# Performance work log

Measured on AMD Instinct MI355X. Metric: run time of the kernel, lower is better.

Reference implementation:

```python
import jax, jax.numpy as jnp
import numpy as np

R = 64          # n_rois
B = 128         # batch_size (graphs)
IN = 2048       # voxels per ROI
HID = 512       # max(32, IN//4)
ROI_OUT = 20
G1, G2 = 64, 128
FC1, FC2, OUT = 512, 1024, 6400
N = R * B       # total graph nodes


def _block_complete_edges():
    # per-sample complete directed graph over R ROIs (no self loops)
    r = np.arange(R)
    s, d = np.meshgrid(r, r, indexing='ij')
    m = s != d
    s, d = s[m], d[m]                       # [R*(R-1)]
    off = (np.arange(B) * R)[:, None]       # [B,1]
    src = (s[None, :] + off).reshape(-1)
    dst = (d[None, :] + off).reshape(-1)
    return np.stack([src, dst]).astype(np.int64)  # [2, E]


def setup_inputs() -> dict:
    key = jax.random.key(0)
    ks = jax.random.split(key, 16)
    sd = lambda *s: 1.0 / np.sqrt(s[0])
    inp = {
        'x': jax.random.normal(ks[0], (R, B * IN), jnp.float32),
        'edge_index': jnp.asarray(_block_complete_edges()),
        'batch': jnp.repeat(jnp.arange(B, dtype=jnp.int64), R),
        # per-ROI MLP params (batched over ROI axis)
        'W1': jax.random.normal(ks[1], (R, IN, HID), jnp.float32) * sd(IN),
        'b1': jnp.zeros((R, HID), jnp.float32),
        'W2': jax.random.normal(ks[2], (R, HID, ROI_OUT), jnp.float32) * sd(HID),
        'b2': jnp.zeros((R, ROI_OUT), jnp.float32),
        # GCN params
        'Wg1': jax.random.normal(ks[3], (ROI_OUT, G1), jnp.float32) * sd(ROI_OUT),
        'bg1': jnp.zeros((G1,), jnp.float32),
        'Wg2': jax.random.normal(ks[4], (G1, G2), jnp.float32) * sd(G1),
        'bg2': jnp.zeros((G2,), jnp.float32),
        # FC stack
        'Wf1': jax.random.normal(ks[5], (G2, FC1), jnp.float32) * sd(G2),
        'bf1': jnp.zeros((FC1,), jnp.float32),
        'Wf2': jax.random.normal(ks[6], (FC1, FC2), jnp.float32) * sd(FC1),
        'bf2': jnp.zeros((FC2,), jnp.float32),
        'Wo': jax.random.normal(ks[7], (FC2, OUT), jnp.float32) * sd(FC2),
        'bo': jnp.zeros((OUT,), jnp.float32),
    }
    return inp


def _gcn(h, src, dst, W, b):
    # PyG GCNConv: symmetric norm with self loops, then linear
    loop = jnp.arange(N)
    s = jnp.concatenate([src, loop])
    d = jnp.concatenate([dst, loop])
    deg = jax.ops.segment_sum(jnp.ones(s.shape[0], h.dtype), d, num_segments=N)
    dinv = jax.lax.rsqrt(deg)  # deg >= 1 due to self loops
    hw = h @ W                                  # [N, out]
    msg = hw[s] * (dinv[s] * dinv[d])[:, None]  # [E+N, out]
    return jax.ops.segment_sum(msg, d, num_segments=N) + b


def reference(x, edge_index, batch, W1, b1, W2, b2, Wg1, bg1, Wg2, bg2,
              Wf1, bf1, Wf2, bf2, Wo, bo):
    # per-ROI MLPs, batched: x[r] holds B contiguous chunks of IN voxels
    xr = x.reshape(R, B, IN)
    h = jax.nn.relu(jnp.einsum('rbi,rih->rbh', xr, W1) + b1[:, None, :])
    f = jnp.einsum('rbh,rho->rbo', h, W2) + b2[:, None, :]   # [R,B,ROI_OUT]
    # node order in torch code: for b: for r -> node = b*R + r
    node_feats = f.transpose(1, 0, 2).reshape(N, ROI_OUT)

    src, dst = edge_index[0], edge_index[1]
    g = jax.nn.relu(_gcn(node_feats, src, dst, Wg1, bg1))
    g = jax.nn.relu(_gcn(g, src, dst, Wg2, bg2))

    # global mean pool over each graph's R nodes
    pooled = jax.ops.segment_sum(g, batch, num_segments=B) / R  # [B, G2]

    y = jax.nn.relu(pooled @ Wf1 + bf1)
    y = jax.nn.relu(y @ Wf2 + bf2)
    return y @ Wo + bo  # [B, OUT]
```

## Files before the change

kernel.cpp:

```cpp
#include <hip/hip_runtime.h>
#include <hip/hip_bf16.h>
#include <cstdint>

typedef float  f32x4 __attribute__((ext_vector_type(4)));
typedef short  s16x4 __attribute__((ext_vector_type(4)));
typedef short  s16x8 __attribute__((ext_vector_type(8)));
typedef __bf16 bf16x8 __attribute__((ext_vector_type(8)));
typedef unsigned int u32x2 __attribute__((ext_vector_type(2)));
typedef unsigned int u32x4 __attribute__((ext_vector_type(4)));

static __device__ __forceinline__ unsigned short f2bf(float f) {
  union { float f; unsigned u; } v; v.f = f;
  unsigned r = v.u + 0x7fffu + ((v.u >> 16) & 1u);
  return (unsigned short)(r >> 16);
}

static __device__ __forceinline__ unsigned pk2(float lo, float hi) {
  unsigned r;
  asm("v_cvt_pk_bf16_f32 %0, %1, %2" : "=v"(r) : "v"(lo), "v"(hi));
  return r;
}

static __device__ __forceinline__ f32x4 mfma16(bf16x8 a, bf16x8 b, f32x4 c) {
  return __builtin_amdgcn_mfma_f32_16x16x32_bf16(a, b, c, 0, 0, 0);
}

__global__ __launch_bounds__(512, 4)
void k_mlp(const float* __restrict__ X, const float* __restrict__ W1,
           const float* __restrict__ b1, const float* __restrict__ W2,
           float* __restrict__ m1)
{
  __shared__ short smem[21760];
  __shared__ float biasS[128];
  short* const lds_a  = smem;
  short* const lds_b  = smem + 9216;
  short* const lds_h  = smem;
  short* const lds_w2 = smem + 17408;

  const int bid = blockIdx.x;
  const int r = (bid & 7) + ((bid >> 5) << 3);
  const int c = (bid >> 3) & 3;

  const float* xr = X + (long)r * (128 * 2048);
  const float* wr = W1 + (long)r * (2048 * 512) + c * 128;
  const float* bp = b1 + (long)r * 512 + c * 128;

  const int t = threadIdx.x;
  const int lane = t & 63;
  const int w = t >> 6;

  if (t < 128) biasS[t] = bp[t];

  const int aRow = t >> 2;
  const int aCol = (t & 3) * 4;
  const int bn   = t & 127;
  const int bk0  = (t >> 7) * 8;

  f32x4 aR[4];
  float bR[2][8];

  auto loadTile = [&](int ks) {
    const float* xp = xr + (long)aRow * 2048 + ks * 64 + aCol;
#pragma unroll
    for (int j = 0; j < 4; j++)
      aR[j] = *(const f32x4*)(xp + 16 * j);
    const float* wp = wr + (long)(ks * 64 + bk0) * 512 + bn;
#pragma unroll
    for (int g = 0; g < 2; g++)
#pragma unroll
      for (int j = 0; j < 8; j++)
        bR[g][j] = wp[(long)(g * 32 + j) * 512];
  };

  auto storeTile = [&]() {
#pragma unroll
    for (int j = 0; j < 4; j++) {
      u32x2 v;
      v[0] = pk2(aR[j][0], aR[j][1]);
      v[1] = pk2(aR[j][2], aR[j][3]);
      *(u32x2*)&lds_a[aRow * 72 + aCol + 16 * j] = v;
    }
#pragma unroll
    for (int g = 0; g < 2; g++) {
      u32x4 v;
      v[0] = pk2(bR[g][0], bR[g][1]);
      v[1] = pk2(bR[g][2], bR[g][3]);
      v[2] = pk2(bR[g][4], bR[g][5]);
      v[3] = pk2(bR[g][6], bR[g][7]);
      *(u32x4*)&lds_b[bn * 72 + bk0 + g * 32] = v;
    }
  };

  const int wm = w & 1, wn = w >> 1;
  const int mBase = wm * 64, nBase = wn * 32;
  const int lm = lane & 15, lg = lane >> 4;

  f32x4 acc[4][2];
#pragma unroll
  for (int i = 0; i < 4; i++)
#pragma unroll
    for (int j = 0; j < 2; j++) acc[i][j] = f32x4{0.f, 0.f, 0.f, 0.f};

  loadTile(0);
  for (int ks = 0; ks < 32; ks++) {
    __syncthreads();
    storeTile();
    __syncthreads();
    if (ks + 1 < 32) loadTile(ks + 1);
    bf16x8 af[2][4], bfr[2][2];
#pragma unroll
    for (int g = 0; g < 2; g++) {
#pragma unroll
      for (int i = 0; i < 4; i++)
        af[g][i] = *(const bf16x8*)&lds_a[(mBase + i * 16 + lm) * 72 + g * 32 + lg * 8];
#pragma unroll
      for (int j = 0; j < 2; j++)
        bfr[g][j] = *(const bf16x8*)&lds_b[(nBase + j * 16 + lm) * 72 + g * 32 + lg * 8];
    }
#pragma unroll
    for (int mi = 0; mi < 4; mi++)
#pragma unroll
      for (int ni = 0; ni < 2; ni++) {
        acc[mi][ni] = mfma16(af[0][mi], bfr[0][ni], acc[mi][ni]);
        acc[mi][ni] = mfma16(af[1][mi], bfr[1][ni], acc[mi][ni]);
      }
  }

  __syncthreads();

#pragma unroll
  for (int mi = 0; mi < 4; mi++)
#pragma unroll
    for (int ni = 0; ni < 2; ni++) {
      const int col = nBase + ni * 16 + lm;
      const float bv = biasS[col];
#pragma unroll
      for (int i = 0; i < 4; i++) {
        const int row = mBase + mi * 16 + lg * 4 + i;
        float v = acc[mi][ni][i] + bv;
        v = v > 0.f ? v : 0.f;
        lds_h[row * 136 + col] = (short)f2bf(v);
      }
    }
  {
    const float* w2r = W2 + (long)r * (512 * 20) + (long)(c * 128) * 20;
#pragma unroll
    for (int i = 0; i < 8; i++) {
      const int idx = t * 8 + i;
      const int o = idx >> 7, kh = idx & 127;
      const float v = (o < 20) ? w2r[(long)kh * 20 + o] : 0.f;
      lds_w2[o * 136 + kh] = (short)f2bf(v);
    }
  }
  __syncthreads();
  f32x4 acc2[2];
  acc2[0] = f32x4{0.f, 0.f, 0.f, 0.f};
  acc2[1] = f32x4{0.f, 0.f, 0.f, 0.f};
#pragma unroll
  for (int ks2 = 0; ks2 < 4; ks2++) {
    bf16x8 a0 = *(const bf16x8*)&lds_h[(w * 16 + lm) * 136 + ks2 * 32 + lg * 8];
    bf16x8 b0 = *(const bf16x8*)&lds_w2[lm * 136 + ks2 * 32 + lg * 8];
    bf16x8 b1v = *(const bf16x8*)&lds_w2[(16 + lm) * 136 + ks2 * 32 + lg * 8];
    acc2[0] = mfma16(a0, b0, acc2[0]);
    acc2[1] = mfma16(a0, b1v, acc2[1]);
  }
#pragma unroll
  for (int ni = 0; ni < 2; ni++)
#pragma unroll
    for (int i = 0; i < 4; i++) {
      const int m = w * 16 + lg * 4 + i;
      const int o = ni * 16 + lm;
      if (o < 20)
        atomicAdd(&m1[m * 20 + o], acc2[ni][i] * (1.f / 64.f));
    }
}

template<int RELU>
__global__ __launch_bounds__(256)
void gemm_n64(const float* __restrict__ X, int ldx,
              const float* __restrict__ W, int ldw,
              const float* __restrict__ bias,
              float* __restrict__ out, int ldo, int kSteps)
{
  __shared__ short lds_a[128 * 72];
  __shared__ short lds_b[64 * 72];
  __shared__ float biasS[64];

  const int c = blockIdx.x;
  const int t = threadIdx.x;
  const int lane = t & 63;
  const int w = t >> 6;

  if (t < 64) biasS[t] = bias[c * 64 + t];

  const int aRow = t >> 2;
  const int aCol = (t & 3) * 4;
  const int bn   = t & 63;
  const int bk0  = w * 8;

  f32x4 aR[2][4];
  float bR[2][8];

  auto loadTile = [&](int ks) {
    const float* xp = X + (long)aRow * ldx + ks * 64 + aCol;
#pragma unroll
    for (int j = 0; j < 4; j++) {
      aR[0][j] = *(const f32x4*)(xp + 16 * j);
      aR[1][j] = *(const f32x4*)(xp + (long)64 * ldx + 16 * j);
    }
    const float* wp = W + (long)(ks * 64 + bk0) * ldw + c * 64 + bn;
#pragma unroll
    for (int g = 0; g < 2; g++)
#pragma unroll
      for (int j = 0; j < 8; j++)
        bR[g][j] = wp[(long)(g * 32 + j) * ldw];
  };

  auto storeTile = [&]() {
#pragma unroll
    for (int g = 0; g < 2; g++)
#pragma unroll
      for (int j = 0; j < 4; j++) {
        u32x2 v;
        v[0] = pk2(aR[g][j][0], aR[g][j][1]);
        v[1] = pk2(aR[g][j][2], aR[g][j][3]);
        *(u32x2*)&lds_a[(aRow + 64 * g) * 72 + aCol + 16 * j] = v;
      }
#pragma unroll
    for (int g = 0; g < 2; g++) {
      u32x4 v;
      v[0] = pk2(bR[g][0], bR[g][1]);
      v[1] = pk2(bR[g][2], bR[g][3]);
      v[2] = pk2(bR[g][4], bR[g][5]);
      v[3] = pk2(bR[g][6], bR[g][7]);
      *(u32x4*)&lds_b[bn * 72 + bk0 + g * 32] = v;
    }
  };

  const int wm = w & 1, wn = w >> 1;
  const int mBase = wm * 64, nBase = wn * 32;
  const int lm = lane & 15, lg = lane >> 4;

  f32x4 acc[4][2];
#pragma unroll
  for (int i = 0; i < 4; i++)
#pragma unroll
    for (int j = 0; j < 2; j++) acc[i][j] = f32x4{0.f, 0.f, 0.f, 0.f};

  loadTile(0);
  for (int ks = 0; ks < kSteps; ks++) {
    __syncthreads();
    storeTile();
    __syncthreads();
    if (ks + 1 < kSteps) loadTile(ks + 1);
    bf16x8 af[2][4], bfr[2][2];
#pragma unroll
    for (int g = 0; g < 2; g++) {
#pragma unroll
      for (int i = 0; i < 4; i++)
        af[g][i] = *(const bf16x8*)&lds_a[(mBase + i * 16 + lm) * 72 + g * 32 + lg * 8];
#pragma unroll
      for (int j = 0; j < 2; j++)
        bfr[g][j] = *(const bf16x8*)&lds_b[(nBase + j * 16 + lm) * 72 + g * 32 + lg * 8];
    }
#pragma unroll
    for (int mi = 0; mi < 4; mi++)
#pragma unroll
      for (int ni = 0; ni < 2; ni++) {
        acc[mi][ni] = mfma16(af[0][mi], bfr[0][ni], acc[mi][ni]);
        acc[mi][ni] = mfma16(af[1][mi], bfr[1][ni], acc[mi][ni]);
      }
  }

  float* outp = out + c * 64;
#pragma unroll
  for (int mi = 0; mi < 4; mi++)
#pragma unroll
    for (int ni = 0; ni < 2; ni++) {
      const int col = nBase + ni * 16 + lm;
      const float bv = biasS[col];
#pragma unroll
      for (int i = 0; i < 4; i++) {
        const int row = mBase + mi * 16 + lg * 4 + i;
        float v = acc[mi][ni][i] + bv;
        if (RELU) v = v > 0.f ? v : 0.f;
        outp[(long)row * ldo + col] = v;
      }
    }
}

__global__ void k_init_m1(const float* __restrict__ b2, float* __restrict__ m1) {
  const int i = blockIdx.x * blockDim.x + threadIdx.x;
  if (i >= 128 * 20) return;
  const int o = i % 20;
  float s = 0.f;
  for (int r = 0; r < 64; r++) s += b2[r * 20 + o];
  m1[i] = s * (1.f / 64.f);
}

template<int K, int RELU>
__global__ void k_fc_small(const float* __restrict__ in, const float* __restrict__ Wt,
                           const float* __restrict__ bias, float* __restrict__ out,
                           int N)
{
  const int i = blockIdx.x * blockDim.x + threadIdx.x;
  const int b = i / N;
  if (b >= 128) return;
  const int j = i - b * N;
  float s = bias[j];
  const float* ip = in + (long)b * K;
#pragma unroll
  for (int k = 0; k < K; k++) s += ip[k] * Wt[k * N + j];
  out[i] = (RELU && s < 0.f) ? 0.f : s;
}

extern "C" void kernel_launch(void* const* d_in, const int* in_sizes, int n_in,
                              void* d_out, int out_size, void* d_ws, size_t ws_size,
                              hipStream_t stream)
{
  const float* x   = (const float*)d_in[0];
  const float* W1  = (const float*)d_in[3];
  const float* b1  = (const float*)d_in[4];
  const float* W2  = (const float*)d_in[5];
  const float* b2  = (const float*)d_in[6];
  const float* Wg1 = (const float*)d_in[7];
  const float* bg1 = (const float*)d_in[8];
  const float* Wg2 = (const float*)d_in[9];
  const float* bg2 = (const float*)d_in[10];
  const float* Wf1 = (const float*)d_in[11];
  const float* bf1 = (const float*)d_in[12];
  const float* Wf2 = (const float*)d_in[13];
  const float* bf2 = (const float*)d_in[14];
  const float* Wo  = (const float*)d_in[15];
  const float* bo  = (const float*)d_in[16];
  float* out = (float*)d_out;

  float* ws = (float*)d_ws;
  float* m1 = ws;
  float* g1 = ws + 4096;
  float* g2 = ws + 16384;
  float* y1 = ws + 32768;
  float* y2 = ws + 98304;

  k_init_m1<<<10, 256, 0, stream>>>(b2, m1);
  k_mlp<<<256, 512, 0, stream>>>(x, W1, b1, W2, m1);
  k_fc_small<20, 1><<<32, 256, 0, stream>>>(m1, Wg1, bg1, g1, 64);
  k_fc_small<64, 1><<<64, 256, 0, stream>>>(g1, Wg2, bg2, g2, 128);
  gemm_n64<1><<<8,   256, 0, stream>>>(g2, 128,  Wf1, 512,  bf1, y1, 512, 2);
  gemm_n64<1><<<16,  256, 0, stream>>>(y1, 512,  Wf2, 1024, bf2, y2, 1024, 8);
  gemm_n64<0><<<100, 256, 0, stream>>>(y2, 1024, Wo,  6400, bo,  out, 6400, 16);
}
```

Measured before the change: 501.0 us.

## Double-buffer global tile prefetch in registers for per-ROI MLP GEMM

Prefetches two K-tiles ahead into two alternating register buffers instead of one, so global load latency gets more compute to hide behind. The loop is unrolled by two and alternates buffers. To fit the extra registers, the minimum-blocks-per-CU hint is dropped from launch bounds, which may cut occupancy.

```diff
diff --git a/kernel.cpp b/kernel.cpp
--- a/kernel.cpp
+++ b/kernel.cpp
@@ -25,7 +25,7 @@
   return __builtin_amdgcn_mfma_f32_16x16x32_bf16(a, b, c, 0, 0, 0);
 }
 
-__global__ __launch_bounds__(512, 4)
+__global__ __launch_bounds__(512)
 void k_mlp(const float* __restrict__ X, const float* __restrict__ W1,
            const float* __restrict__ b1, const float* __restrict__ W2,
            float* __restrict__ m1)
@@ -56,37 +56,37 @@
   const int bn   = t & 127;
   const int bk0  = (t >> 7) * 8;
 
-  f32x4 aR[4];
-  float bR[2][8];
-
-  auto loadTile = [&](int ks) {
+  f32x4 aR0[4], aR1[4];
+  float bR0[2][8], bR1[2][8];
+
+  auto loadTile = [&](int ks, f32x4 (&aS)[4], float (&bS)[2][8]) {
     const float* xp = xr + (long)aRow * 2048 + ks * 64 + aCol;
 #pragma unroll
     for (int j = 0; j < 4; j++)
-      aR[j] = *(const f32x4*)(xp + 16 * j);
+      aS[j] = *(const f32x4*)(xp + 16 * j);
     const float* wp = wr + (long)(ks * 64 + bk0) * 512 + bn;
 #pragma unroll
     for (int g = 0; g < 2; g++)
 #pragma unroll
       for (int j = 0; j < 8; j++)
-        bR[g][j] = wp[(long)(g * 32 + j) * 512];
-  };
-
-  auto storeTile = [&]() {
+        bS[g][j] = wp[(long)(g * 32 + j) * 512];
+  };
+
+  auto storeTile = [&](f32x4 (&aS)[4], float (&bS)[2][8]) {
 #pragma unroll
     for (int j = 0; j < 4; j++) {
       u32x2 v;
-      v[0] = pk2(aR[j][0], aR[j][1]);
-      v[1] = pk2(aR[j][2], aR[j][3]);
+      v[0] = pk2(aS[j][0], aS[j][1]);
+      v[1] = pk2(aS[j][2], aS[j][3]);
       *(u32x2*)&lds_a[aRow * 72 + aCol + 16 * j] = v;
     }
 #pragma unroll
     for (int g = 0; g < 2; g++) {
       u32x4 v;
-      v[0] = pk2(bR[g][0], bR[g][1]);
-      v[1] = pk2(bR[g][2], bR[g][3]);
-      v[2] = pk2(bR[g][4], bR[g][5]);
-      v[3] = pk2(bR[g][6], bR[g][7]);
+      v[0] = pk2(bS[g][0], bS[g][1]);
+      v[1] = pk2(bS[g][2], bS[g][3]);
+      v[2] = pk2(bS[g][4], bS[g][5]);
+      v[3] = pk2(bS[g][6], bS[g][7]);
       *(u32x4*)&lds_b[bn * 72 + bk0 + g * 32] = v;
     }
   };
@@ -101,12 +101,7 @@
 #pragma unroll
     for (int j = 0; j < 2; j++) acc[i][j] = f32x4{0.f, 0.f, 0.f, 0.f};
 
-  loadTile(0);
-  for (int ks = 0; ks < 32; ks++) {
-    __syncthreads();
-    storeTile();
-    __syncthreads();
-    if (ks + 1 < 32) loadTile(ks + 1);
+  auto compute = [&]() {
     bf16x8 af[2][4], bfr[2][2];
 #pragma unroll
     for (int g = 0; g < 2; g++) {
@@ -124,6 +119,21 @@
         acc[mi][ni] = mfma16(af[0][mi], bfr[0][ni], acc[mi][ni]);
         acc[mi][ni] = mfma16(af[1][mi], bfr[1][ni], acc[mi][ni]);
       }
+  };
+
+  loadTile(0, aR0, bR0);
+  loadTile(1, aR1, bR1);
+  for (int ks = 0; ks < 32; ks += 2) {
+    __syncthreads();
+    storeTile(aR0, bR0);
+    __syncthreads();
+    if (ks + 2 < 32) loadTile(ks + 2, aR0, bR0);
+    compute();
+    __syncthreads();
+    storeTile(aR1, bR1);
+    __syncthreads();
+    if (ks + 3 < 32) loadTile(ks + 3, aR1, bR1);
+    compute();
   }
 
   __syncthreads();
```

Result: no change. 495.6 us (-1.1%).
